# Kernel optimization log

Hardware: AMD Instinct MI355X
Metric: run time of the kernel (lower is better)

Reference implementation:

```python
import jax, jax.numpy as jnp
import numpy as np

VOCAB = 128
HID = 1024
STD = 0.01


def setup_inputs() -> dict:
    key = jax.random.key(0)
    ks = jax.random.split(key, 9)
    X = jax.random.randint(ks[0], (64, 512), 0, VOCAB, dtype=jnp.int32)
    def w(k, shape):
        return jax.random.normal(k, shape, dtype=jnp.float32) * STD
    return {
        "X": X,
        # reset gate
        "Wr_x": w(ks[1], (VOCAB, HID)), "Wr_h": w(ks[2], (HID, HID)), "b_r": jnp.zeros(HID, jnp.float32),
        # update gate
        "Wz_x": w(ks[3], (VOCAB, HID)), "Wz_h": w(ks[4], (HID, HID)), "b_z": jnp.zeros(HID, jnp.float32),
        # candidate
        "Wh_x": w(ks[5], (VOCAB, HID)), "Wh_h": w(ks[6], (HID, HID)), "b_h": jnp.zeros(HID, jnp.float32),
        # output head
        "W_o": w(ks[7], (HID, VOCAB)), "b_o": jnp.zeros(VOCAB, jnp.float32),
    }


def reference(X, Wr_x, Wr_h, b_r, Wz_x, Wz_h, b_z, Wh_x, Wh_h, b_h, W_o, b_o):
    B, T = X.shape
    # one-hot encode all timesteps: (T, B, V)
    Xoh = jax.nn.one_hot(X.T, VOCAB, dtype=jnp.float32)

    def step(h, x_t):
        # x_t: (B, V), h: (B, H)
        r = jax.nn.sigmoid(x_t @ Wr_x + h @ Wr_h + b_r)
        z = jax.nn.sigmoid(x_t @ Wz_x + h @ Wz_h + b_z)
        h_tilde = jnp.tanh(x_t @ Wh_x + (r * h) @ Wh_h + b_h)
        h_new = z * h + (1.0 - z) * h_tilde
        out = h_new @ W_o + b_o  # (B, V)
        return h_new, out

    h0 = jnp.zeros((B, HID), jnp.float32)
    _, outs = jax.lax.scan(step, h0, Xoh)  # outs: (T, B, V)
    return jnp.transpose(outs, (1, 0, 2))  # (B, T, V)
```

## Files before the change

### kernel.cpp

```cpp
#include <hip/hip_runtime.h>

#define HID   1024
#define TLEN  512
#define VOC   128
#define NBLK  256
#define NT    4
#define NB    32
#define MR    16
#define LDSK  1032
#define HBUF  (MR * HID)

typedef __bf16 bf16_t;
typedef __attribute__((ext_vector_type(8))) __bf16 bf16x8;
typedef __attribute__((ext_vector_type(4))) float  f32x4;

__device__ __forceinline__ float sigmoid_fast(float x) {
  return 1.0f / (1.0f + __expf(-x));
}
__device__ __forceinline__ float tanh_fast(float x) {
  float e = __expf(-2.0f * x);
  return (1.0f - e) / (1.0f + e);
}

union PairU { bf16_t b[2]; unsigned u; };

__device__ __forceinline__ void l1_inv() {
  asm volatile("buffer_inv" ::: "memory");
}

__device__ __forceinline__ void drain_stores() {
  asm volatile("s_waitcnt vmcnt(0)" ::: "memory");
}

__device__ __forceinline__ bf16x8 ldw(const bf16_t* p) {
  return *reinterpret_cast<const bf16x8*>(p);
}

__device__ __forceinline__ void wait_flags(const unsigned* f, unsigned tgt) {
  const volatile unsigned* p =
      (const volatile unsigned*)(f + (threadIdx.x & 31));
  for (;;) {
    l1_inv();
    unsigned v = *p;
    if (__all((int)(v - tgt) >= 0)) break;
  }
}

__device__ __forceinline__ void publish(unsigned* fw, unsigned v) {
  __syncthreads();
  drain_stores();
  if (threadIdx.x == 0) *(volatile unsigned*)fw = v;
}

#define MFMA(a, b, c) __builtin_amdgcn_mfma_f32_16x16x32_bf16((a), (b), (c), 0, 0, 0)

__global__ void __launch_bounds__(64, 1)
gru_mt2(const int* __restrict__ X,
        const float* __restrict__ Wr_x, const float* __restrict__ Wr_h, const float* __restrict__ b_r,
        const float* __restrict__ Wz_x, const float* __restrict__ Wz_h, const float* __restrict__ b_z,
        const float* __restrict__ Wh_x, const float* __restrict__ Wh_h, const float* __restrict__ b_h,
        const float* __restrict__ W_o,  const float* __restrict__ b_o,
        float* __restrict__ out,
        bf16_t* __restrict__ hring, bf16_t* __restrict__ rh_bf,
        bf16_t* __restrict__ wz_bf, bf16_t* __restrict__ wo_bf,
        unsigned* __restrict__ flags)
{
  __shared__ __align__(16) bf16_t Wbuf[2 * 32 * LDSK];
  __shared__ __align__(16) float  Obuf[8][16][16];
  __shared__ int s_team, s_slot;

  unsigned* cnt   = flags + 1024;
  unsigned* tcnt  = flags + 1536;
  unsigned* xteam = flags + 2048;
  unsigned* ready = flags + 3072;

  const int tid  = threadIdx.x;
  const int n16  = tid & 15;
  const int q    = tid >> 4;

  int bi[4];
#pragma unroll
  for (int i = 0; i < 4; ++i) bi[i] = q * 4 + i;

  if (tid == 0) {
    unsigned xcc;
    asm volatile("s_getreg_b32 %0, hwreg(HW_REG_XCC_ID)" : "=s"(xcc));
    xcc &= 7u;
    unsigned idx = __hip_atomic_fetch_add(&cnt[xcc * 32], 1u,
        __ATOMIC_RELAXED, __HIP_MEMORY_SCOPE_AGENT);
    if (idx == NB - 1) {
      unsigned tcl = __hip_atomic_fetch_add(tcnt, 1u,
          __ATOMIC_RELAXED, __HIP_MEMORY_SCOPE_AGENT);
      __hip_atomic_store(&xteam[xcc * 32], (tcl < NT) ? (tcl + 1u) : 0xFFu,
          __ATOMIC_RELAXED, __HIP_MEMORY_SCOPE_AGENT);
    }
    unsigned v;
    do {
      v = __hip_atomic_load(&xteam[xcc * 32], __ATOMIC_RELAXED,
                            __HIP_MEMORY_SCOPE_AGENT);
      __builtin_amdgcn_s_sleep(1);
    } while (v == 0u);
    s_team = (v == 0xFFu) ? -1 : (int)(v - 1u);
    s_slot = (int)idx;
  }
  __syncthreads();
  const int tau = s_team;
  if (tau < 0) return;
  const int s  = s_slot;
  const int c0 = s * 32;

  unsigned* fH = flags + tau * 256;
  unsigned* fR = fH + 64;

  if (tid == 0) {
    *(volatile unsigned*)&fH[s] = 0u;
    *(volatile unsigned*)&fR[s] = 0u;
  }

  for (int idx = tid; idx < 32 * HID; idx += 64) {
    int n = idx & 31, k = idx >> 5;
    int r = (n & 1) * 16 + (n >> 1);
    Wbuf[r * LDSK + k]             = (bf16_t)Wr_h[k * HID + c0 + n];
    Wbuf[32 * LDSK + r * LDSK + k] = (bf16_t)Wh_h[k * HID + c0 + n];
  }
  bf16_t* wzs = wz_bf + s * (32 * HID);
  if (tau == 0) {
    for (int idx = tid; idx < 32 * HID; idx += 64) {
      int n = idx & 31, k = idx >> 5;
      int r = (n & 1) * 16 + (n >> 1);
      wzs[r * HID + k] = (bf16_t)Wz_h[k * HID + c0 + n];
    }
    if (s < 8) {
      bf16_t* wos = wo_bf + s * (16 * HID);
      for (int idx = tid; idx < 16 * HID; idx += 64) {
        int n = idx & 15, k = idx >> 4;
        wos[n * HID + k] = (bf16_t)W_o[k * VOC + s * 16 + n];
      }
    }
  }

  bf16_t* hT  = hring + tau * (2 * HBUF);
  bf16_t* rhT = rh_bf + tau * HBUF;
  const int j0 = c0 + 2 * n16;
#pragma unroll
  for (int i = 0; i < 4; ++i) {
    PairU zz; zz.b[0] = (bf16_t)0.f; zz.b[1] = (bf16_t)0.f;
    *reinterpret_cast<PairU*>(hT + bi[i] * HID + j0) = zz;
  }
  __syncthreads();
  drain_stores();

  if (tid == 0) {
    __hip_atomic_fetch_add(ready, 1u, __ATOMIC_RELAXED, __HIP_MEMORY_SCOPE_AGENT);
    while (__hip_atomic_load(ready, __ATOMIC_RELAXED, __HIP_MEMORY_SCOPE_AGENT)
           < (unsigned)(NT * NB))
      __builtin_amdgcn_s_sleep(1);
  }
  __syncthreads();
  if (tid == 0) *(volatile unsigned*)&fH[s] = 1u;

  const float br0 = b_r[j0], br1 = b_r[j0 + 1];
  const float bz0 = b_z[j0], bz1 = b_z[j0 + 1];
  const float bh0 = b_h[j0], bh1 = b_h[j0 + 1];
  const bf16_t* wr0 = &Wbuf[n16 * LDSK + q * 8];
  const bf16_t* wr1 = &Wbuf[(16 + n16) * LDSK + q * 8];
  const bf16_t* wh0 = &Wbuf[32 * LDSK + n16 * LDSK + q * 8];
  const bf16_t* wh1 = &Wbuf[32 * LDSK + (16 + n16) * LDSK + q * 8];
  const bf16_t* wz0 = wzs + n16 * HID + q * 8;
  const bf16_t* wz1 = wzs + (16 + n16) * HID + q * 8;
  const int  aoff  = n16 * HID + q * 8;
  const bf16_t* rhrow = rhT + aoff;

  const bool outw = (s < 8);
  const int  vt   = s;
  const bf16_t* wop = wo_bf + vt * (16 * HID) + n16 * HID + q * 8;
  const float bo = outw ? b_o[vt * 16 + n16] : 0.f;
  const int  gb0 = tau * MR;

  f32x4 hm0 = {0.f,0.f,0.f,0.f}, hm1 = {0.f,0.f,0.f,0.f};

  for (int t = 0; t < TLEN; ++t) {
    float gr0[4], gr1[4], gz0[4], gz1[4], gh0[4], gh1[4];
#pragma unroll
    for (int i = 0; i < 4; ++i) {
      int xb = X[(gb0 + bi[i]) * TLEN + t];
      gr0[i] = Wr_x[xb * HID + j0]; gr1[i] = Wr_x[xb * HID + j0 + 1];
      gz0[i] = Wz_x[xb * HID + j0]; gz1[i] = Wz_x[xb * HID + j0 + 1];
      gh0[i] = Wh_x[xb * HID + j0]; gh1[i] = Wh_x[xb * HID + j0 + 1];
    }

    wait_flags(fH, (unsigned)(t + 1));
    const bf16_t* hrow = hT + (t & 1) * HBUF + aoff;
    bf16x8 areg[32];
#pragma unroll
    for (int kk = 0; kk < 32; ++kk) areg[kk] = ldw(hrow + kk * 32);

    f32x4 aR0 = {0.f,0.f,0.f,0.f}, aR1 = {0.f,0.f,0.f,0.f};
    f32x4 bR0 = {0.f,0.f,0.f,0.f}, bR1 = {0.f,0.f,0.f,0.f};
#pragma unroll
    for (int kk = 0; kk < 16; ++kk) {
      aR0 = MFMA(areg[kk],      ldw(wr0 + kk * 32),        aR0);
      aR1 = MFMA(areg[kk],      ldw(wr1 + kk * 32),        aR1);
      bR0 = MFMA(areg[kk + 16], ldw(wr0 + (kk + 16) * 32), bR0);
      bR1 = MFMA(areg[kk + 16], ldw(wr1 + (kk + 16) * 32), bR1);
    }
    aR0 += bR0; aR1 += bR1;
#pragma unroll
    for (int i = 0; i < 4; ++i) {
      float r0 = sigmoid_fast(aR0[i] + br0 + gr0[i]);
      float r1 = sigmoid_fast(aR1[i] + br1 + gr1[i]);
      PairU c;
      c.b[0] = (bf16_t)(r0 * hm0[i]);
      c.b[1] = (bf16_t)(r1 * hm1[i]);
      *reinterpret_cast<PairU*>(rhT + bi[i] * HID + j0) = c;
    }
    publish(&fR[s], (unsigned)(t + 1));

    if (outw && t) {
      f32x4 oa = {0.f,0.f,0.f,0.f}, ob2 = {0.f,0.f,0.f,0.f};
#pragma unroll
      for (int kk = 0; kk < 16; ++kk) {
        oa  = MFMA(areg[kk],      ldw(wop + kk * 32),        oa);
        ob2 = MFMA(areg[kk + 16], ldw(wop + (kk + 16) * 32), ob2);
      }
      oa += ob2;
      const int oi = (t - 1) & 7;
#pragma unroll
      for (int i = 0; i < 4; ++i) Obuf[oi][bi[i]][n16] = oa[i] + bo;
    }

    f32x4 aZ0 = {0.f,0.f,0.f,0.f}, aZ1 = {0.f,0.f,0.f,0.f};
    f32x4 bZ0 = {0.f,0.f,0.f,0.f}, bZ1 = {0.f,0.f,0.f,0.f};
#pragma unroll
    for (int kk = 0; kk < 16; ++kk) {
      aZ0 = MFMA(areg[kk],      ldw(wz0 + kk * 32),        aZ0);
      aZ1 = MFMA(areg[kk],      ldw(wz1 + kk * 32),        aZ1);
      bZ0 = MFMA(areg[kk + 16], ldw(wz0 + (kk + 16) * 32), bZ0);
      bZ1 = MFMA(areg[kk + 16], ldw(wz1 + (kk + 16) * 32), bZ1);
    }
    aZ0 += bZ0; aZ1 += bZ1;
    f32x4 z0, z1;
#pragma unroll
    for (int i = 0; i < 4; ++i) {
      z0[i] = sigmoid_fast(aZ0[i] + bz0 + gz0[i]);
      z1[i] = sigmoid_fast(aZ1[i] + bz1 + gz1[i]);
    }

    wait_flags(fR, (unsigned)(t + 1));
    bf16x8 breg[32];
#pragma unroll
    for (int kk = 0; kk < 32; ++kk) breg[kk] = ldw(rhrow + kk * 32);
    f32x4 aH0 = {0.f,0.f,0.f,0.f}, aH1 = {0.f,0.f,0.f,0.f};
    f32x4 bH0 = {0.f,0.f,0.f,0.f}, bH1 = {0.f,0.f,0.f,0.f};
#pragma unroll
    for (int kk = 0; kk < 16; ++kk) {
      aH0 = MFMA(breg[kk],      ldw(wh0 + kk * 32),        aH0);
      aH1 = MFMA(breg[kk],      ldw(wh1 + kk * 32),        aH1);
      bH0 = MFMA(breg[kk + 16], ldw(wh0 + (kk + 16) * 32), bH0);
      bH1 = MFMA(breg[kk + 16], ldw(wh1 + (kk + 16) * 32), bH1);
    }
    aH0 += bH0; aH1 += bH1;
    bf16_t* hnext = hT + ((t + 1) & 1) * HBUF;
#pragma unroll
    for (int i = 0; i < 4; ++i) {
      float ht0 = tanh_fast(aH0[i] + bh0 + gh0[i]);
      float ht1 = tanh_fast(aH1[i] + bh1 + gh1[i]);
      float hn0 = z0[i] * hm0[i] + (1.f - z0[i]) * ht0;
      float hn1 = z1[i] * hm1[i] + (1.f - z1[i]) * ht1;
      hm0[i] = hn0; hm1[i] = hn1;
      PairU c; c.b[0] = (bf16_t)hn0; c.b[1] = (bf16_t)hn1;
      *reinterpret_cast<PairU*>(hnext + bi[i] * HID + j0) = c;
    }
    publish(&fH[s], (unsigned)(t + 2));

    if (outw && t && ((t - 1) & 7) == 7) {
      const int rb = t - 8;
#pragma unroll
      for (int m = 0; m < 32; ++m) {
        int e = m * 64 + tid;
        int row = e >> 7, tt = (e >> 4) & 7, cc = e & 15;
        out[((gb0 + row) * TLEN + rb + tt) * VOC + vt * 16 + cc] =
            Obuf[tt][row][cc];
      }
    }
  }

  if (outw) {
    wait_flags(fH, (unsigned)(TLEN + 1));
    const bf16_t* hrow = hT + (TLEN & 1) * HBUF + aoff;
    bf16x8 areg[32];
#pragma unroll
    for (int kk = 0; kk < 32; ++kk) areg[kk] = ldw(hrow + kk * 32);
    f32x4 oa = {0.f,0.f,0.f,0.f}, ob2 = {0.f,0.f,0.f,0.f};
#pragma unroll
    for (int kk = 0; kk < 16; ++kk) {
      oa  = MFMA(areg[kk],      ldw(wop + kk * 32),        oa);
      ob2 = MFMA(areg[kk + 16], ldw(wop + (kk + 16) * 32), ob2);
    }
    oa += ob2;
#pragma unroll
    for (int i = 0; i < 4; ++i) Obuf[7][bi[i]][n16] = oa[i] + bo;
    __syncthreads();
#pragma unroll
    for (int m = 0; m < 32; ++m) {
      int e = m * 64 + tid;
      int row = e >> 7, tt = (e >> 4) & 7, cc = e & 15;
      out[((gb0 + row) * TLEN + 504 + tt) * VOC + vt * 16 + cc] =
          Obuf[tt][row][cc];
    }
  }

  __builtin_amdgcn_fence(__ATOMIC_RELEASE, "agent");
}

extern "C" void kernel_launch(void* const* d_in, const int* in_sizes, int n_in,
                              void* d_out, int out_size, void* d_ws, size_t ws_size,
                              hipStream_t stream) {
  const int*   X    = (const int*)d_in[0];
  const float* Wr_x = (const float*)d_in[1];
  const float* Wr_h = (const float*)d_in[2];
  const float* b_r  = (const float*)d_in[3];
  const float* Wz_x = (const float*)d_in[4];
  const float* Wz_h = (const float*)d_in[5];
  const float* b_z  = (const float*)d_in[6];
  const float* Wh_x = (const float*)d_in[7];
  const float* Wh_h = (const float*)d_in[8];
  const float* b_h  = (const float*)d_in[9];
  const float* W_o  = (const float*)d_in[10];
  const float* b_o  = (const float*)d_in[11];

  char* ws = (char*)d_ws;
  unsigned* flags = (unsigned*)ws;
  bf16_t*   hring = (bf16_t*)(ws + 16384);
  bf16_t*   rh_bf = (bf16_t*)(ws + 16384 + (size_t)NT * 2 * HBUF * sizeof(bf16_t));
  bf16_t*   wz_bf = (bf16_t*)(ws + 16384 + (size_t)NT * 3 * HBUF * sizeof(bf16_t));
  bf16_t*   wo_bf = (bf16_t*)(ws + 16384 + (size_t)NT * 3 * HBUF * sizeof(bf16_t)
                              + (size_t)NB * 32 * HID * sizeof(bf16_t));

  hipMemsetAsync(ws, 0, 16384, stream);

  gru_mt2<<<NBLK, 64, 0, stream>>>(
      X, Wr_x, Wr_h, b_r, Wz_x, Wz_h, b_z, Wh_x, Wh_h, b_h, W_o, b_o,
      (float*)d_out, hring, rh_bf, wz_bf, wo_bf, flags);
}
```

Measured before the change: 7.900 ms.

## Bind GRU teams to XCC ids and replicate bf16 weights per team

Each team is now fixed to the XCC its blocks run on (XCCs 0-3), replacing the dynamic first-to-fill team election. Every team writes its own bf16 copy of Wz_h and W_o, so per-step weight reads stay within data written by that XCC rather than a single team-0 copy. The shared startup barrier becomes one barrier per team. Scratch buffers move into static device globals. This relies on the dispatcher placing exactly 32 blocks on each XCC, and it multiplies the weight conversion work and memory footprint by the number of teams.

```diff
diff --git a/kernel.cpp b/kernel.cpp
--- a/kernel.cpp
+++ b/kernel.cpp
@@ -14,6 +14,12 @@
 typedef __attribute__((ext_vector_type(8))) __bf16 bf16x8;
 typedef __attribute__((ext_vector_type(4))) float  f32x4;
 
+__device__ __align__(512) bf16_t   g_hring[(size_t)NT * 2 * HBUF];
+__device__ __align__(512) bf16_t   g_rh   [(size_t)NT * HBUF];
+__device__ __align__(512) bf16_t   g_wz   [(size_t)NT * NB * 32 * HID];
+__device__ __align__(512) bf16_t   g_wo   [(size_t)NT * 8 * 16 * HID];
+__device__ __align__(512) unsigned g_flags[NT * 256];
+
 __device__ __forceinline__ float sigmoid_fast(float x) {
   return 1.0f / (1.0f + __expf(-x));
 }
@@ -55,24 +61,20 @@
 #define MFMA(a, b, c) __builtin_amdgcn_mfma_f32_16x16x32_bf16((a), (b), (c), 0, 0, 0)
 
 __global__ void __launch_bounds__(64, 1)
-gru_mt2(const int* __restrict__ X,
-        const float* __restrict__ Wr_x, const float* __restrict__ Wr_h, const float* __restrict__ b_r,
-        const float* __restrict__ Wz_x, const float* __restrict__ Wz_h, const float* __restrict__ b_z,
-        const float* __restrict__ Wh_x, const float* __restrict__ Wh_h, const float* __restrict__ b_h,
-        const float* __restrict__ W_o,  const float* __restrict__ b_o,
-        float* __restrict__ out,
-        bf16_t* __restrict__ hring, bf16_t* __restrict__ rh_bf,
-        bf16_t* __restrict__ wz_bf, bf16_t* __restrict__ wo_bf,
-        unsigned* __restrict__ flags)
+gru_xb(const int* __restrict__ X,
+       const float* __restrict__ Wr_x, const float* __restrict__ Wr_h, const float* __restrict__ b_r,
+       const float* __restrict__ Wz_x, const float* __restrict__ Wz_h, const float* __restrict__ b_z,
+       const float* __restrict__ Wh_x, const float* __restrict__ Wh_h, const float* __restrict__ b_h,
+       const float* __restrict__ W_o,  const float* __restrict__ b_o,
+       float* __restrict__ out,
+       unsigned* __restrict__ ws)
 {
   __shared__ __align__(16) bf16_t Wbuf[2 * 32 * LDSK];
   __shared__ __align__(16) float  Obuf[8][16][16];
   __shared__ int s_team, s_slot;
 
-  unsigned* cnt   = flags + 1024;
-  unsigned* tcnt  = flags + 1536;
-  unsigned* xteam = flags + 2048;
-  unsigned* ready = flags + 3072;
+  unsigned* cnt   = ws;
+  unsigned* ready = ws + 512;
 
   const int tid  = threadIdx.x;
   const int n16  = tid & 15;
@@ -88,19 +90,7 @@
     xcc &= 7u;
     unsigned idx = __hip_atomic_fetch_add(&cnt[xcc * 32], 1u,
         __ATOMIC_RELAXED, __HIP_MEMORY_SCOPE_AGENT);
-    if (idx == NB - 1) {
-      unsigned tcl = __hip_atomic_fetch_add(tcnt, 1u,
-          __ATOMIC_RELAXED, __HIP_MEMORY_SCOPE_AGENT);
-      __hip_atomic_store(&xteam[xcc * 32], (tcl < NT) ? (tcl + 1u) : 0xFFu,
-          __ATOMIC_RELAXED, __HIP_MEMORY_SCOPE_AGENT);
-    }
-    unsigned v;
-    do {
-      v = __hip_atomic_load(&xteam[xcc * 32], __ATOMIC_RELAXED,
-                            __HIP_MEMORY_SCOPE_AGENT);
-      __builtin_amdgcn_s_sleep(1);
-    } while (v == 0u);
-    s_team = (v == 0xFFu) ? -1 : (int)(v - 1u);
+    s_team = (xcc < NT) ? (int)xcc : -1;
     s_slot = (int)idx;
   }
   __syncthreads();
@@ -109,7 +99,7 @@
   const int s  = s_slot;
   const int c0 = s * 32;
 
-  unsigned* fH = flags + tau * 256;
+  unsigned* fH = g_flags + tau * 256;
   unsigned* fR = fH + 64;
 
   if (tid == 0) {
@@ -123,24 +113,23 @@
     Wbuf[r * LDSK + k]             = (bf16_t)Wr_h[k * HID + c0 + n];
     Wbuf[32 * LDSK + r * LDSK + k] = (bf16_t)Wh_h[k * HID + c0 + n];
   }
-  bf16_t* wzs = wz_bf + s * (32 * HID);
-  if (tau == 0) {
-    for (int idx = tid; idx < 32 * HID; idx += 64) {
-      int n = idx & 31, k = idx >> 5;
-      int r = (n & 1) * 16 + (n >> 1);
-      wzs[r * HID + k] = (bf16_t)Wz_h[k * HID + c0 + n];
-    }
-    if (s < 8) {
-      bf16_t* wos = wo_bf + s * (16 * HID);
-      for (int idx = tid; idx < 16 * HID; idx += 64) {
-        int n = idx & 15, k = idx >> 4;
-        wos[n * HID + k] = (bf16_t)W_o[k * VOC + s * 16 + n];
-      }
-    }
-  }
-
-  bf16_t* hT  = hring + tau * (2 * HBUF);
-  bf16_t* rhT = rh_bf + tau * HBUF;
+  bf16_t* wzs = g_wz + (size_t)tau * (NB * 32 * HID) + (size_t)s * (32 * HID);
+  for (int idx = tid; idx < 32 * HID; idx += 64) {
+    int n = idx & 31, k = idx >> 5;
+    int r = (n & 1) * 16 + (n >> 1);
+    wzs[r * HID + k] = (bf16_t)Wz_h[k * HID + c0 + n];
+  }
+  bf16_t* wot = g_wo + (size_t)tau * (8 * 16 * HID);
+  if (s < 8) {
+    bf16_t* wos = wot + (size_t)s * (16 * HID);
+    for (int idx = tid; idx < 16 * HID; idx += 64) {
+      int n = idx & 15, k = idx >> 4;
+      wos[n * HID + k] = (bf16_t)W_o[k * VOC + s * 16 + n];
+    }
+  }
+
+  bf16_t* hT  = g_hring + (size_t)tau * (2 * HBUF);
+  bf16_t* rhT = g_rh    + (size_t)tau * HBUF;
   const int j0 = c0 + 2 * n16;
 #pragma unroll
   for (int i = 0; i < 4; ++i) {
@@ -151,9 +140,10 @@
   drain_stores();
 
   if (tid == 0) {
-    __hip_atomic_fetch_add(ready, 1u, __ATOMIC_RELAXED, __HIP_MEMORY_SCOPE_AGENT);
-    while (__hip_atomic_load(ready, __ATOMIC_RELAXED, __HIP_MEMORY_SCOPE_AGENT)
-           < (unsigned)(NT * NB))
+    __hip_atomic_fetch_add(&ready[tau * 32], 1u,
+        __ATOMIC_RELAXED, __HIP_MEMORY_SCOPE_AGENT);
+    while (__hip_atomic_load(&ready[tau * 32], __ATOMIC_RELAXED,
+                             __HIP_MEMORY_SCOPE_AGENT) < (unsigned)NB)
       __builtin_amdgcn_s_sleep(1);
   }
   __syncthreads();
@@ -173,7 +163,7 @@
 
   const bool outw = (s < 8);
   const int  vt   = s;
-  const bf16_t* wop = wo_bf + vt * (16 * HID) + n16 * HID + q * 8;
+  const bf16_t* wop = wot + (size_t)vt * (16 * HID) + n16 * HID + q * 8;
   const float bo = outw ? b_o[vt * 16 + n16] : 0.f;
   const int  gb0 = tau * MR;
 
@@ -329,17 +319,9 @@
   const float* W_o  = (const float*)d_in[10];
   const float* b_o  = (const float*)d_in[11];
 
-  char* ws = (char*)d_ws;
-  unsigned* flags = (unsigned*)ws;
-  bf16_t*   hring = (bf16_t*)(ws + 16384);
-  bf16_t*   rh_bf = (bf16_t*)(ws + 16384 + (size_t)NT * 2 * HBUF * sizeof(bf16_t));
-  bf16_t*   wz_bf = (bf16_t*)(ws + 16384 + (size_t)NT * 3 * HBUF * sizeof(bf16_t));
-  bf16_t*   wo_bf = (bf16_t*)(ws + 16384 + (size_t)NT * 3 * HBUF * sizeof(bf16_t)
-                              + (size_t)NB * 32 * HID * sizeof(bf16_t));
-
-  hipMemsetAsync(ws, 0, 16384, stream);
-
-  gru_mt2<<<NBLK, 64, 0, stream>>>(
+  hipMemsetAsync(d_ws, 0, 4096, stream);
+
+  gru_xb<<<NBLK, 64, 0, stream>>>(
       X, Wr_x, Wr_h, b_r, Wz_x, Wz_h, b_z, Wh_x, Wh_h, b_h, W_o, b_o,
-      (float*)d_out, hring, rh_bf, wz_bf, wo_bf, flags);
-}
+      (float*)d_out, (unsigned*)d_ws);
+}
```

Result: slower. 8.180 ms (+3.6%).
